# Kernel tuning notes

Hardware: AMD Instinct MI355X
Metric: run time of the kernel (lower is better)

Reference implementation:

```python
import jax, jax.numpy as jnp
import numpy as np

B, SQ, SK, D, H, DFF, L = 8, 1024, 1024, 512, 8, 2048, 2
HD = D // H  # head dim = 64
EPS = 1e-5


def _ln(x, g, b):
    mu = jnp.mean(x, axis=-1, keepdims=True)
    var = jnp.mean((x - mu) ** 2, axis=-1, keepdims=True)
    return (x - mu) * jax.lax.rsqrt(var + EPS) * g + b


def setup_inputs() -> dict:
    key = jax.random.key(0)
    ks = jax.random.split(key, 16)
    std = 0.02
    inp = {
        'q': jax.random.normal(ks[0], (B, SQ, D), jnp.float32),
        'k': jax.random.normal(ks[1], (B, SK, D), jnp.float32),
        'v': jax.random.normal(ks[2], (B, SK, D), jnp.float32),
        # per-layer stacked params (weights stored [in, out])
        'WQ': jax.random.normal(ks[3], (L, D, D), jnp.float32) * std,
        'bQ': jnp.zeros((L, D), jnp.float32),
        'WK': jax.random.normal(ks[4], (L, D, D), jnp.float32) * std,
        'bK': jnp.zeros((L, D), jnp.float32),
        'WV': jax.random.normal(ks[5], (L, D, D), jnp.float32) * std,
        'bV': jnp.zeros((L, D), jnp.float32),
        'WO': jax.random.normal(ks[6], (L, D, D), jnp.float32) * std,
        'bO': jnp.zeros((L, D), jnp.float32),
        'Wf1': jax.random.normal(ks[7], (L, D, DFF), jnp.float32) * std,
        'bf1': jnp.zeros((L, DFF), jnp.float32),
        'Wf2': jax.random.normal(ks[8], (L, DFF, D), jnp.float32) * std,
        'bf2': jnp.zeros((L, D), jnp.float32),
        'ln1_g': jnp.ones((L, D), jnp.float32),
        'ln1_b': jnp.zeros((L, D), jnp.float32),
        'ln2_g': jnp.ones((L, D), jnp.float32),
        'ln2_b': jnp.zeros((L, D), jnp.float32),
        'scale': jnp.full((L,), HD ** -0.5, jnp.float32),       # self.scale init
        'extra_scale': jnp.ones((L,), jnp.float32),             # self.extra_scale init
        'gate_attn': jnp.ones((L,), jnp.float32),
        'gate_ffn': jnp.ones((L,), jnp.float32),
    }
    return inp


def reference(q, k, v, WQ, bQ, WK, bK, WV, bV, WO, bO, Wf1, bf1, Wf2, bf2,
              ln1_g, ln1_b, ln2_g, ln2_b, scale, extra_scale, gate_attn, gate_ffn):
    prev = None  # Realformer residual attention scores
    for i in range(L):
        # QKV projections -> [B, H, S, HD]
        qh = (jnp.einsum('bsd,de->bse', q, WQ[i]) + bQ[i]).reshape(B, SQ, H, HD).transpose(0, 2, 1, 3)
        kh = (jnp.einsum('bsd,de->bse', k, WK[i]) + bK[i]).reshape(B, SK, H, HD).transpose(0, 2, 1, 3)
        vh = (jnp.einsum('bsd,de->bse', v, WV[i]) + bV[i]).reshape(B, SK, H, HD).transpose(0, 2, 1, 3)
        eff_scale = scale[i] * jnp.clip(extra_scale[i], 0.01, 50.0)
        scores = jnp.einsum('bhqd,bhkd->bhqk', qh, kh) * eff_scale  # [B,H,SQ,SK]
        if prev is not None:
            scores = scores + prev
        attn = jax.nn.softmax(scores, axis=-1)
        out = jnp.einsum('bhqk,bhkd->bhqd', attn, vh)
        out = out.transpose(0, 2, 1, 3).reshape(B, SQ, D)
        out = jnp.einsum('bsd,de->bse', out, WO[i]) + bO[i]
        # gated residual + post-norm
        q = q + jax.nn.softplus(gate_attn[i]) * out
        q = _ln(q, ln1_g[i], ln1_b[i])
        # FFN (exact gelu like torch default)
        ff = jax.nn.gelu(jnp.einsum('bsd,df->bsf', q, Wf1[i]) + bf1[i], approximate=False)
        ff = jnp.einsum('bsf,fd->bsd', ff, Wf2[i]) + bf2[i]
        q = q + jax.nn.softplus(gate_ffn[i]) * ff
        q = _ln(q, ln2_g[i], ln2_b[i])
        prev = scores
    return q
```

## Files before the change

### kernel.cpp

```cpp
#include <hip/hip_runtime.h>

#define B_   8
#define SQ_  1024
#define SK_  1024
#define D_   512
#define H_   8
#define DFF_ 2048
#define L_   2
#define HD_  64
#define M_   8192

typedef __bf16 bf16;
using bf16x8 = __attribute__((ext_vector_type(8))) __bf16;
using f32x4  = __attribute__((ext_vector_type(4))) float;

__device__ inline f32x4 mfma16(bf16x8 a, bf16x8 b, f32x4 c) {
  return __builtin_amdgcn_mfma_f32_16x16x32_bf16(a, b, c, 0, 0, 0);
}

__device__ __forceinline__ void gl2lds16(const bf16* g, bf16* l) {
  __builtin_amdgcn_global_load_lds(
      (const __attribute__((address_space(1))) void*)g,
      (__attribute__((address_space(3))) void*)l, 16, 0, 0);
}

__device__ __forceinline__ float gelu_fast(float x) {
  float u = 1.5957691216f * (x + 0.044715f * x * x * x);
  return x / (1.0f + __expf(-u));
}

struct TP4 { const float* in[4]; bf16* out[4]; };
__global__ __launch_bounds__(256) void transpose4_k(TP4 p) {
  __shared__ bf16 tile[32][33];
  int z = blockIdx.z, wsel = z >> 1, l = z & 1;
  const float* inp  = p.in[wsel]  + (size_t)l * D_ * D_;
  bf16*        outp = p.out[wsel] + (size_t)l * D_ * D_;
  int c0 = blockIdx.x * 32, r0 = blockIdx.y * 32;
  int tx = threadIdx.x & 31, ty = threadIdx.x >> 5;
#pragma unroll
  for (int i = 0; i < 32; i += 8)
    tile[ty + i][tx] = (bf16)inp[(size_t)(r0 + ty + i) * D_ + c0 + tx];
  __syncthreads();
#pragma unroll
  for (int i = 0; i < 32; i += 8)
    outp[(size_t)(c0 + ty + i) * D_ + r0 + tx] = tile[tx][ty + i];
}

__global__ __launch_bounds__(256) void transpose_k(
    const float* __restrict__ in, bf16* __restrict__ out, int R, int C) {
  __shared__ bf16 tile[32][33];
  const float* inp  = in  + (size_t)blockIdx.z * R * C;
  bf16*        outp = out + (size_t)blockIdx.z * R * C;
  int c0 = blockIdx.x * 32, r0 = blockIdx.y * 32;
  int tx = threadIdx.x & 31, ty = threadIdx.x >> 5;
#pragma unroll
  for (int i = 0; i < 32; i += 8)
    tile[ty + i][tx] = (bf16)inp[(size_t)(r0 + ty + i) * C + c0 + tx];
  __syncthreads();
#pragma unroll
  for (int i = 0; i < 32; i += 8)
    outp[(size_t)(c0 + ty + i) * R + r0 + tx] = tile[tx][ty + i];
}

__global__ __launch_bounds__(256) void f2b3_k(
    const float* __restrict__ a, const float* __restrict__ b,
    const float* __restrict__ c, bf16* __restrict__ oa,
    bf16* __restrict__ ob, bf16* __restrict__ oc) {
  int which = blockIdx.y;
  const float* in = (which == 0) ? a : (which == 1) ? b : c;
  bf16* out = (which == 0) ? oa : (which == 1) ? ob : oc;
  int i = (blockIdx.x * 256 + threadIdx.x) * 4;
  float4 v = *(const float4*)&in[i];
  out[i] = (bf16)v.x; out[i + 1] = (bf16)v.y;
  out[i + 2] = (bf16)v.z; out[i + 3] = (bf16)v.w;
}

struct G256 { const bf16* A; const bf16* Bt; const float* bias; bf16* C; };

#define MFB(mh) \
  _Pragma("unroll") \
  for (int mi = 0; mi < 4; mi++) { \
    _Pragma("unroll") \
    for (int ni = 0; ni < 4; ni++) \
      acc[(mh) * 4 + mi][ni] = mfma16(a[mi], b[ni], acc[(mh) * 4 + mi][ni]); \
  }

#define PHASE(s, mh, STAGE, VM) \
  { \
    if ((mh) == 0) { \
      a[0] = ldA(s, 0); a[1] = ldA(s, 1); a[2] = ldA(s, 2); a[3] = ldA(s, 3); \
      b[0] = ldB(s, 0); b[1] = ldB(s, 1); b[2] = ldB(s, 2); b[3] = ldB(s, 3); \
    } else { \
      a[0] = ldA(s, 4); a[1] = ldA(s, 5); a[2] = ldA(s, 6); a[3] = ldA(s, 7); \
    } \
    STAGE; \
    VM; \
    __builtin_amdgcn_s_barrier(); \
    asm volatile("s_waitcnt lgkmcnt(0)" ::: "memory"); \
    __builtin_amdgcn_sched_barrier(0); \
    __builtin_amdgcn_s_setprio(1); \
    MFB(mh); \
    __builtin_amdgcn_s_setprio(0); \
    __builtin_amdgcn_s_barrier(); \
  }

__global__ __launch_bounds__(512, 2) void gemm256_k(G256 g0, G256 g1,
                                                    int Nsz, int Ksz,
                                                    int gelu) {
  __shared__ bf16 As[4 * 8192];
  __shared__ bf16 Bs[4 * 8192];
  const G256 g = blockIdx.z ? g1 : g0;
  const int tid = threadIdx.x;
  const int w = tid >> 6, lane = tid & 63;
  const int quad = lane >> 4, l16 = lane & 15;
  const int wm = w >> 2, wn = w & 3;
  const int m0 = blockIdx.x * 256, n0 = blockIdx.y * 256;
  const int NCH = Ksz >> 5;
  const int ITERS = NCH >> 2;

  const int srow = tid >> 2;
  const int ssw = ((tid & 3) ^ (srow & 3) ^ ((srow >> 2) & 3)) << 3;
  const int swr = ((quad ^ (l16 & 3) ^ (l16 >> 2)) << 3);

  auto stageA = [&](int kc, int s) {
    const bf16* gp = g.A + (size_t)(m0 + srow) * Ksz + kc * 32 + ssw;
    gl2lds16(gp, &As[s * 8192 + w * 512]);
    gl2lds16(gp + (size_t)128 * Ksz, &As[s * 8192 + 4096 + w * 512]);
  };
  auto stageB = [&](int kc, int s) {
    const bf16* gp = g.Bt + (size_t)(n0 + srow) * Ksz + kc * 32 + ssw;
    gl2lds16(gp, &Bs[s * 8192 + w * 512]);
    gl2lds16(gp + (size_t)128 * Ksz, &Bs[s * 8192 + 4096 + w * 512]);
  };
  auto ldA = [&](int s, int mi) {
    return *(const bf16x8*)&As[s * 8192 + (wm * 128 + mi * 16 + l16) * 32 + swr];
  };
  auto ldB = [&](int s, int ni) {
    return *(const bf16x8*)&Bs[s * 8192 + (wn * 64 + ni * 16 + l16) * 32 + swr];
  };

  f32x4 acc[8][4] = {};

  stageA(0, 0); stageB(0, 0);
  stageA(1, 1); stageB(1, 1);
  stageA(2, 2); stageB(2, 2);
  asm volatile("s_waitcnt vmcnt(4)" ::: "memory");
  __builtin_amdgcn_s_barrier();

  for (int it = 0; it < ITERS; ++it) {
    const int c = it * 4;
    const bool last = (it + 1 == ITERS);
    bf16x8 a[4], b[4];
    PHASE(0, 0, stageA(c + 3, 3), )
    PHASE(0, 1, stageB(c + 3, 3), )
    PHASE(1, 0, if (!last) stageA(c + 4, 0), )
    PHASE(1, 1, if (!last) stageB(c + 4, 0),
          if (!last) { asm volatile("s_waitcnt vmcnt(4)" ::: "memory"); }
          else { asm volatile("s_waitcnt vmcnt(0)" ::: "memory"); })
    PHASE(2, 0, if (!last) stageA(c + 5, 1), )
    PHASE(2, 1, if (!last) stageB(c + 5, 1), )
    PHASE(3, 0, if (!last) stageA(c + 6, 2), )
    PHASE(3, 1, if (!last) stageB(c + 6, 2),
          asm volatile("s_waitcnt vmcnt(4)" ::: "memory"))
  }

#pragma unroll
  for (int mi = 0; mi < 8; mi++)
#pragma unroll
    for (int ni = 0; ni < 4; ni++) {
      const int col = n0 + wn * 64 + ni * 16 + l16;
      const float bv = g.bias[col];
#pragma unroll
      for (int r = 0; r < 4; r++) {
        const int row = m0 + wm * 128 + mi * 16 + quad * 4 + r;
        float x = acc[mi][ni][r] + bv;
        if (gelu) x = gelu_fast(x);
        g.C[(size_t)row * Nsz + col] = (bf16)x;
      }
    }
}

__global__ __launch_bounds__(512, 2) void gemm128_k(
    const bf16* __restrict__ A, const bf16* __restrict__ Bt,
    const float* __restrict__ bias, bf16* __restrict__ Cb,
    float* __restrict__ Cf, int Nsz, int Ksz) {
  __shared__ bf16 As[4 * 4096];
  __shared__ bf16 Bs[4 * 4096];
  const int tid = threadIdx.x;
  const int w = tid >> 6, lane = tid & 63;
  const int quad = lane >> 4, l16 = lane & 15;
  const int wm = w >> 2, wn = w & 3;
  const int m0 = blockIdx.x * 128, n0 = blockIdx.y * 128;
  const int NCH = Ksz >> 5;

  const int srow = tid >> 2;
  const int ssw = ((tid & 3) ^ (srow & 3) ^ ((srow >> 2) & 3)) << 3;
  const int swr = ((quad ^ (l16 & 3) ^ (l16 >> 2)) << 3);

  auto stageChunk = [&](int kc) {
    const int s = kc & 3;
    gl2lds16(A + (size_t)(m0 + srow) * Ksz + kc * 32 + ssw,
             &As[s * 4096 + w * 512]);
    gl2lds16(Bt + (size_t)(n0 + srow) * Ksz + kc * 32 + ssw,
             &Bs[s * 4096 + w * 512]);
  };
  auto ldA = [&](int s, int mi) {
    return *(const bf16x8*)&As[s * 4096 + (wm * 64 + mi * 16 + l16) * 32 + swr];
  };
  auto ldB = [&](int s, int ni) {
    return *(const bf16x8*)&Bs[s * 4096 + (wn * 32 + ni * 16 + l16) * 32 + swr];
  };

  f32x4 acc[4][2] = {};

  stageChunk(0); stageChunk(1); stageChunk(2);
  asm volatile("s_waitcnt vmcnt(4)" ::: "memory");
  __builtin_amdgcn_s_barrier();

  auto phase = [&](int c, int vml) {
    const int s = c & 3;
    if (vml == 4) stageChunk(c + 3);
    bf16x8 a0 = ldA(s, 0), a1 = ldA(s, 1), a2 = ldA(s, 2), a3 = ldA(s, 3);
    bf16x8 b0 = ldB(s, 0), b1 = ldB(s, 1);
    if (vml == 4)      asm volatile("s_waitcnt vmcnt(4)" ::: "memory");
    else if (vml == 2) asm volatile("s_waitcnt vmcnt(2)" ::: "memory");
    else if (vml == 0) asm volatile("s_waitcnt vmcnt(0)" ::: "memory");
    __builtin_amdgcn_s_barrier();
    asm volatile("s_waitcnt lgkmcnt(0)" ::: "memory");
    __builtin_amdgcn_sched_barrier(0);
    __builtin_amdgcn_s_setprio(1);
    acc[0][0] = mfma16(a0, b0, acc[0][0]);
    acc[0][1] = mfma16(a0, b1, acc[0][1]);
    acc[1][0] = mfma16(a1, b0, acc[1][0]);
    acc[1][1] = mfma16(a1, b1, acc[1][1]);
    acc[2][0] = mfma16(a2, b0, acc[2][0]);
    acc[2][1] = mfma16(a2, b1, acc[2][1]);
    acc[3][0] = mfma16(a3, b0, acc[3][0]);
    acc[3][1] = mfma16(a3, b1, acc[3][1]);
    __builtin_amdgcn_s_setprio(0);
    __builtin_amdgcn_s_barrier();
  };

  for (int c = 0; c + 4 <= NCH; ++c) phase(c, 4);
  phase(NCH - 3, 2);
  phase(NCH - 2, 0);
  phase(NCH - 1, -1);

#pragma unroll
  for (int mi = 0; mi < 4; mi++)
#pragma unroll
    for (int ni = 0; ni < 2; ni++) {
      const int col = n0 + wn * 32 + ni * 16 + l16;
      const float bv = bias[col];
#pragma unroll
      for (int r = 0; r < 4; r++) {
        const int row = m0 + wm * 64 + mi * 16 + quad * 4 + r;
        float x = acc[mi][ni][r] + bv;
        size_t idx = (size_t)row * Nsz + col;
        if (Cb) Cb[idx] = (bf16)x;
        if (Cf) Cf[idx] = x;
      }
    }
}

__global__ __launch_bounds__(256) void vtrans2_k(const bf16* __restrict__ vhh,
                                                 bf16* __restrict__ vt0,
                                                 bf16* __restrict__ vt1) {
  __shared__ bf16 sm[64][72];
  int kt = blockIdx.x, bh = blockIdx.y, z = blockIdx.z;
  int coloff = z ? D_ : 0;
  bf16* vt = z ? vt1 : vt0;
  int b = bh >> 3, h = bh & 7;
  int tid = threadIdx.x;
  for (int c = tid; c < 512; c += 256) {
    int key = c >> 3, off = (c & 7) * 8;
    *(uint4*)&sm[key][off] = *(const uint4*)
        &vhh[(size_t)(b * SK_ + kt * 64 + key) * (2 * D_) + coloff + h * 64 + off];
  }
  __syncthreads();
  for (int c = tid; c < 512; c += 256) {
    int hd = c >> 3, koff = (c & 7) * 8;
    bf16 tmp[8];
#pragma unroll
    for (int j = 0; j < 8; j++) tmp[j] = sm[koff + j][hd];
    *(uint4*)&vt[(size_t)(bh * 64 + hd) * SK_ + kt * 64 + koff] = *(uint4*)tmp;
  }
}

template<bool HAS0>
__global__ __launch_bounds__(256) void attn_t(
    const bf16* __restrict__ qh, const bf16* __restrict__ qh0,
    const bf16* __restrict__ kh, const bf16* __restrict__ kh0, int kstride,
    const bf16* __restrict__ vt, const float* __restrict__ scale,
    const float* __restrict__ extra, int li, bf16* __restrict__ ctx) {
  __shared__ bf16 Ks[2 * 2 * 2048];
  __shared__ bf16 K0s[HAS0 ? 2 * 2 * 2048 : 64];
  __shared__ bf16 Vs[2 * 2 * 2048];
  __shared__ bf16 Ps[4][16 * 72];
  int qt = blockIdx.x, bh = blockIdx.y;
  int b = bh >> 3, h = bh & 7;
  int tid = threadIdx.x, w = tid >> 6, lane = tid & 63;
  int quad = lane >> 4, l16 = lane & 15;
  const int r4 = lane >> 2, c4 = (lane & 3) * 8;
  float eff1 = scale[li] * fminf(fmaxf(extra[li], 0.01f), 50.0f);
  float eff0 = HAS0 ? scale[li - 1] * fminf(fmaxf(extra[li - 1], 0.01f), 50.0f) : 0.f;
  bf16x8 aq[2][2], aq0[2][2];
#pragma unroll
  for (int mi = 0; mi < 2; mi++) {
    int qrow = b * SQ_ + qt * 128 + w * 32 + mi * 16 + l16;
    const bf16* qp = qh + (size_t)qrow * D_ + h * 64 + quad * 8;
    aq[mi][0] = *(const bf16x8*)qp; aq[mi][1] = *(const bf16x8*)(qp + 32);
#pragma unroll
    for (int k2 = 0; k2 < 2; k2++)
#pragma unroll
      for (int j = 0; j < 8; j++)
        aq[mi][k2][j] = (bf16)((float)aq[mi][k2][j] * eff1);
    if constexpr (HAS0) {
      const bf16* qp0 = qh0 + (size_t)qrow * D_ + h * 64 + quad * 8;
      aq0[mi][0] = *(const bf16x8*)qp0; aq0[mi][1] = *(const bf16x8*)(qp0 + 32);
#pragma unroll
      for (int k2 = 0; k2 < 2; k2++)
#pragma unroll
        for (int j = 0; j < 8; j++)
          aq0[mi][k2][j] = (bf16)((float)aq0[mi][k2][j] * eff0);
    }
  }
  bf16x8 ones;
#pragma unroll
  for (int j = 0; j < 8; j++) ones[j] = (bf16)1.0f;

  f32x4 o[2][4] = {};
  f32x4 ol[2] = {};

  auto stage = [&](int kt, int bufi) {
    size_t kg = (size_t)(b * SK_ + kt * 64 + w * 16 + r4) * kstride + h * 64 + c4;
    gl2lds16(&kh[kg],      &Ks[(bufi * 2 + 0) * 2048 + (w * 16) * 32]);
    gl2lds16(&kh[kg + 32], &Ks[(bufi * 2 + 1) * 2048 + (w * 16) * 32]);
    if constexpr (HAS0) {
      gl2lds16(&kh0[kg],      &K0s[(bufi * 2 + 0) * 2048 + (w * 16) * 32]);
      gl2lds16(&kh0[kg + 32], &K0s[(bufi * 2 + 1) * 2048 + (w * 16) * 32]);
    }
    size_t vg = (size_t)(bh * 64 + w * 16 + r4) * SK_ + kt * 64 + c4;
    gl2lds16(&vt[vg],      &Vs[(bufi * 2 + 0) * 2048 + (w * 16) * 32]);
    gl2lds16(&vt[vg + 32], &Vs[(bufi * 2 + 1) * 2048 + (w * 16) * 32]);
  };

  stage(0, 0);
  __syncthreads();
  int buf = 0;
  for (int kt = 0; kt < SK_ / 64; kt++, buf ^= 1) {
    if (kt + 1 < SK_ / 64) stage(kt + 1, buf ^ 1);
    bf16x8 bv[2][4];
#pragma unroll
    for (int kk = 0; kk < 2; kk++)
#pragma unroll
      for (int ni = 0; ni < 4; ni++)
        bv[kk][ni] = *(const bf16x8*)&Vs[kk * 2048 + buf * 4096 +
                                         (ni * 16 + l16) * 32 + quad * 8];
#pragma unroll
    for (int mi = 0; mi < 2; mi++) {
#pragma unroll
      for (int ni = 0; ni < 4; ni++) {
        int ro = (ni * 16 + l16) * 32 + quad * 8;
        f32x4 t = {};
        t = mfma16(aq[mi][0], *(const bf16x8*)&Ks[0 * 2048 + buf * 4096 + ro], t);
        t = mfma16(aq[mi][1], *(const bf16x8*)&Ks[1 * 2048 + buf * 4096 + ro], t);
        if constexpr (HAS0) {
          t = mfma16(aq0[mi][0], *(const bf16x8*)&K0s[0 * 2048 + buf * 4096 + ro], t);
          t = mfma16(aq0[mi][1], *(const bf16x8*)&K0s[1 * 2048 + buf * 4096 + ro], t);
        }
#pragma unroll
        for (int r = 0; r < 4; r++)
          Ps[w][(quad * 4 + r) * 72 + ni * 16 + l16] = (bf16)__expf(t[r]);
      }
#pragma unroll
      for (int kk = 0; kk < 2; kk++) {
        bf16x8 ap = *(const bf16x8*)&Ps[w][l16 * 72 + kk * 32 + quad * 8];
        ol[mi] = mfma16(ap, ones, ol[mi]);
#pragma unroll
        for (int ni = 0; ni < 4; ni++)
          o[mi][ni] = mfma16(ap, bv[kk][ni], o[mi][ni]);
      }
    }
    __syncthreads();
  }
#pragma unroll
  for (int mi = 0; mi < 2; mi++)
#pragma unroll
    for (int ni = 0; ni < 4; ni++)
#pragma unroll
      for (int r = 0; r < 4; r++) {
        int row = b * SQ_ + qt * 128 + w * 32 + mi * 16 + quad * 4 + r;
        ctx[(size_t)row * D_ + h * 64 + ni * 16 + l16] =
            (bf16)(o[mi][ni][r] / ol[mi][r]);
      }
}

__global__ __launch_bounds__(256) void ln_k(
    const float* __restrict__ cur_in, const float* __restrict__ add,
    const float* __restrict__ gate, const float* __restrict__ g,
    const float* __restrict__ bb, float* __restrict__ outf,
    bf16* __restrict__ outb) {
  int row = blockIdx.x, tid = threadIdx.x;
  float gv = gate[0];
  float sp = gv > 20.f ? gv : log1pf(expf(gv));
  size_t base = (size_t)row * D_;
  int c0 = tid * 2;
  float2 c2 = *(const float2*)&cur_in[base + c0];
  float2 a2 = *(const float2*)&add[base + c0];
  float x0 = c2.x + sp * a2.x, x1 = c2.y + sp * a2.y;
  float s = x0 + x1, s2 = x0 * x0 + x1 * x1;
#pragma unroll
  for (int m = 1; m < 64; m <<= 1) {
    s += __shfl_xor(s, m);
    s2 += __shfl_xor(s2, m);
  }
  __shared__ float sa[4], sb[4];
  int w = tid >> 6;
  if ((tid & 63) == 0) { sa[w] = s; sb[w] = s2; }
  __syncthreads();
  s = sa[0] + sa[1] + sa[2] + sa[3];
  s2 = sb[0] + sb[1] + sb[2] + sb[3];
  float mu = s * (1.f / D_);
  float var = s2 * (1.f / D_) - mu * mu;
  float rs = rsqrtf(var + 1e-5f);
  float y0 = (x0 - mu) * rs * g[c0] + bb[c0];
  float y1 = (x1 - mu) * rs * g[c0 + 1] + bb[c0 + 1];
  if (outf) { float2 y; y.x = y0; y.y = y1; *(float2*)&outf[base + c0] = y; }
  if (outb) { outb[base + c0] = (bf16)y0; outb[base + c0 + 1] = (bf16)y1; }
}

extern "C" void kernel_launch(void* const* d_in, const int* in_sizes, int n_in,
                              void* d_out, int out_size, void* d_ws,
                              size_t ws_size, hipStream_t stream) {
  const float* qin = (const float*)d_in[0];
  const float* kin = (const float*)d_in[1];
  const float* vin = (const float*)d_in[2];
  const float* WQ  = (const float*)d_in[3];
  const float* bQ  = (const float*)d_in[4];
  const float* WK  = (const float*)d_in[5];
  const float* bK  = (const float*)d_in[6];
  const float* WV  = (const float*)d_in[7];
  const float* bV  = (const float*)d_in[8];
  const float* WO  = (const float*)d_in[9];
  const float* bO  = (const float*)d_in[10];
  const float* Wf1 = (const float*)d_in[11];
  const float* bf1 = (const float*)d_in[12];
  const float* Wf2 = (const float*)d_in[13];
  const float* bf2 = (const float*)d_in[14];
  const float* l1g = (const float*)d_in[15];
  const float* l1b = (const float*)d_in[16];
  const float* l2g = (const float*)d_in[17];
  const float* l2b = (const float*)d_in[18];
  const float* sc  = (const float*)d_in[19];
  const float* ex  = (const float*)d_in[20];
  const float* ga  = (const float*)d_in[21];
  const float* gf  = (const float*)d_in[22];

  char* p = (char*)d_ws;
  auto alloc = [&](size_t bytes) {
    void* r = (void*)p;
    p += (bytes + 255) & ~(size_t)255;
    return r;
  };
  bf16* WQt  = (bf16*)alloc((size_t)L_ * D_ * D_ * 2);
  bf16* WKt  = (bf16*)alloc((size_t)L_ * D_ * D_ * 2);
  bf16* WVt  = (bf16*)alloc((size_t)L_ * D_ * D_ * 2);
  bf16* WOt  = (bf16*)alloc((size_t)L_ * D_ * D_ * 2);
  bf16* Wf1t = (bf16*)alloc((size_t)L_ * D_ * DFF_ * 2);
  bf16* Wf2t = (bf16*)alloc((size_t)L_ * D_ * DFF_ * 2);
  float* cur  = (float*)alloc((size_t)M_ * D_ * 4);
  bf16* curb  = (bf16*)alloc((size_t)M_ * D_ * 2);
  bf16* qb    = (bf16*)alloc((size_t)M_ * D_ * 2);
  bf16* kb    = (bf16*)alloc((size_t)M_ * D_ * 2);
  bf16* vb    = (bf16*)alloc((size_t)M_ * D_ * 2);
  bf16* khh   = (bf16*)alloc((size_t)M_ * 2 * D_ * 2);
  bf16* vhh   = (bf16*)alloc((size_t)M_ * 2 * D_ * 2);
  bf16* qh0b  = (bf16*)alloc((size_t)M_ * D_ * 2);
  bf16* qh1b  = (bf16*)alloc((size_t)M_ * D_ * 2);
  bf16* vt0   = (bf16*)alloc((size_t)M_ * D_ * 2);
  bf16* vt1   = (bf16*)alloc((size_t)M_ * D_ * 2);
  bf16* ctx   = (bf16*)alloc((size_t)M_ * D_ * 2);
  float* proj = (float*)alloc((size_t)M_ * D_ * 4);
  bf16* ffmid = (bf16*)alloc((size_t)M_ * DFF_ * 2);
  float* ffout = (float*)alloc((size_t)M_ * D_ * 4);

  TP4 tp; tp.in[0] = WQ; tp.in[1] = WK; tp.in[2] = WV; tp.in[3] = WO;
  tp.out[0] = WQt; tp.out[1] = WKt; tp.out[2] = WVt; tp.out[3] = WOt;
  transpose4_k<<<dim3(16, 16, 8), 256, 0, stream>>>(tp);
  transpose_k<<<dim3(DFF_ / 32, D_ / 32, L_), 256, 0, stream>>>(Wf1, Wf1t, D_, DFF_);
  transpose_k<<<dim3(D_ / 32, DFF_ / 32, L_), 256, 0, stream>>>(Wf2, Wf2t, DFF_, D_);
  f2b3_k<<<dim3((M_ * D_) / 1024, 3), 256, 0, stream>>>(qin, kin, vin, qb, kb, vb);

  G256 gk; gk.A = kb; gk.Bt = WKt; gk.bias = bK; gk.C = khh;
  G256 gvv; gvv.A = vb; gvv.Bt = WVt; gvv.bias = bV; gvv.C = vhh;
  gemm256_k<<<dim3(M_ / 256, (2 * D_) / 256, 2), 512, 0, stream>>>(
      gk, gvv, 2 * D_, D_, 0);
  vtrans2_k<<<dim3(SK_ / 64, B_ * H_, 2), 256, 0, stream>>>(vhh, vt0, vt1);
  gemm128_k<<<dim3(M_ / 128, 4), 512, 0, stream>>>(
      qb, WQt, bQ, qh0b, nullptr, D_, D_);

  for (int li = 0; li < L_; li++) {
    if (li > 0)
      gemm128_k<<<dim3(M_ / 128, 4), 512, 0, stream>>>(
          curb, WQt + (size_t)li * D_ * D_, bQ + li * D_, qh1b, nullptr, D_, D_);
    if (li == 0)
      attn_t<false><<<dim3(SQ_ / 128, B_ * H_), 256, 0, stream>>>(
          qh0b, qh0b, khh, khh, 2 * D_, vt0, sc, ex, 0, ctx);
    else
      attn_t<true><<<dim3(SQ_ / 128, B_ * H_), 256, 0, stream>>>(
          qh1b, qh0b, khh + (size_t)li * D_, khh, 2 * D_, vt1, sc, ex, 1, ctx);
    gemm128_k<<<dim3(M_ / 128, 4), 512, 0, stream>>>(
        ctx, WOt + (size_t)li * D_ * D_, bO + li * D_, nullptr, proj, D_, D_);
    ln_k<<<M_, 256, 0, stream>>>((li == 0) ? qin : cur, proj, ga + li,
                                 l1g + li * D_, l1b + li * D_, cur, curb);
    G256 gf1; gf1.A = curb; gf1.Bt = Wf1t + (size_t)li * D_ * DFF_;
    gf1.bias = bf1 + li * DFF_; gf1.C = ffmid;
    gemm256_k<<<dim3(M_ / 256, DFF_ / 256, 1), 512, 0, stream>>>(
        gf1, gf1, DFF_, D_, 1);
    gemm128_k<<<dim3(M_ / 128, 4), 512, 0, stream>>>(
        ffmid, Wf2t + (size_t)li * DFF_ * D_, bf2 + li * D_, nullptr, ffout,
        D_, DFF_);
    ln_k<<<M_, 256, 0, stream>>>(cur, ffout, gf + li, l2g + li * D_,
                                 l2b + li * D_,
                                 (li == L_ - 1) ? (float*)d_out : cur,
                                 (li == L_ - 1) ? nullptr : curb);
  }
}
```

Before: 534.9 us.

## Split-K the FFN down-projection with 256 tiles, swizzle attention LDS, add setprio

```diff
diff --git a/kernel.cpp b/kernel.cpp
--- a/kernel.cpp
+++ b/kernel.cpp
@@ -176,6 +176,81 @@
         float x = acc[mi][ni][r] + bv;
         if (gelu) x = gelu_fast(x);
         g.C[(size_t)row * Nsz + col] = (bf16)x;
+      }
+    }
+}
+
+__global__ __launch_bounds__(512, 2) void gemm256s_k(
+    const bf16* __restrict__ A, const bf16* __restrict__ Bt,
+    bf16* __restrict__ P, int Nsz, int Kstride, int Kpart) {
+  __shared__ bf16 As[4 * 8192];
+  __shared__ bf16 Bs[4 * 8192];
+  const int z = blockIdx.z;
+  const int koff = z * Kpart;
+  const int tid = threadIdx.x;
+  const int w = tid >> 6, lane = tid & 63;
+  const int quad = lane >> 4, l16 = lane & 15;
+  const int wm = w >> 2, wn = w & 3;
+  const int m0 = blockIdx.x * 256, n0 = blockIdx.y * 256;
+  const int ITERS = (Kpart >> 5) >> 2;
+
+  const int srow = tid >> 2;
+  const int ssw = ((tid & 3) ^ (srow & 3) ^ ((srow >> 2) & 3)) << 3;
+  const int swr = ((quad ^ (l16 & 3) ^ (l16 >> 2)) << 3);
+
+  auto stageA = [&](int kc, int s) {
+    const bf16* gp = A + (size_t)(m0 + srow) * Kstride + koff + kc * 32 + ssw;
+    gl2lds16(gp, &As[s * 8192 + w * 512]);
+    gl2lds16(gp + (size_t)128 * Kstride, &As[s * 8192 + 4096 + w * 512]);
+  };
+  auto stageB = [&](int kc, int s) {
+    const bf16* gp = Bt + (size_t)(n0 + srow) * Kstride + koff + kc * 32 + ssw;
+    gl2lds16(gp, &Bs[s * 8192 + w * 512]);
+    gl2lds16(gp + (size_t)128 * Kstride, &Bs[s * 8192 + 4096 + w * 512]);
+  };
+  auto ldA = [&](int s, int mi) {
+    return *(const bf16x8*)&As[s * 8192 + (wm * 128 + mi * 16 + l16) * 32 + swr];
+  };
+  auto ldB = [&](int s, int ni) {
+    return *(const bf16x8*)&Bs[s * 8192 + (wn * 64 + ni * 16 + l16) * 32 + swr];
+  };
+
+  f32x4 acc[8][4] = {};
+
+  stageA(0, 0); stageB(0, 0);
+  stageA(1, 1); stageB(1, 1);
+  stageA(2, 2); stageB(2, 2);
+  asm volatile("s_waitcnt vmcnt(4)" ::: "memory");
+  __builtin_amdgcn_s_barrier();
+
+  for (int it = 0; it < ITERS; ++it) {
+    const int c = it * 4;
+    const bool last = (it + 1 == ITERS);
+    bf16x8 a[4], b[4];
+    PHASE(0, 0, stageA(c + 3, 3), )
+    PHASE(0, 1, stageB(c + 3, 3), )
+    PHASE(1, 0, if (!last) stageA(c + 4, 0), )
+    PHASE(1, 1, if (!last) stageB(c + 4, 0),
+          if (!last) { asm volatile("s_waitcnt vmcnt(4)" ::: "memory"); }
+          else { asm volatile("s_waitcnt vmcnt(0)" ::: "memory"); })
+    PHASE(2, 0, if (!last) stageA(c + 5, 1), )
+    PHASE(2, 1, if (!last) stageB(c + 5, 1), )
+    PHASE(3, 0, if (!last) stageA(c + 6, 2), )
+    PHASE(3, 1, if (!last) stageB(c + 6, 2),
+          asm volatile("s_waitcnt vmcnt(4)" ::: "memory"))
+  }
+
+  const size_t Msz = (size_t)gridDim.x * 256;
+  bf16* Pz = P + (size_t)z * Msz * Nsz;
+#pragma unroll
+  for (int mi = 0; mi < 8; mi++)
+#pragma unroll
+    for (int ni = 0; ni < 4; ni++) {
+      const int col = n0 + wn * 64 + ni * 16 + l16;
+#pragma unroll
+      for (int r = 0; r < 4; r++) {
+        const int row = m0 + wm * 128 + mi * 16 + quad * 4 + r;
+        Pz[(size_t)row * Nsz + col] = (bf16)acc[mi][ni][r];
       }
     }
 }
@@ -301,7 +376,9 @@
   int b = bh >> 3, h = bh & 7;
   int tid = threadIdx.x, w = tid >> 6, lane = tid & 63;
   int quad = lane >> 4, l16 = lane & 15;
-  const int r4 = lane >> 2, c4 = (lane & 3) * 8;
+  const int r4 = lane >> 2;
+  const int c4s = (((lane & 3) ^ (r4 & 3) ^ ((r4 >> 2) & 3))) * 8;
+  const int swr = ((quad ^ (l16 & 3) ^ (l16 >> 2)) << 3);
   float eff1 = scale[li] * fminf(fmaxf(extra[li], 0.01f), 50.0f);
   float eff0 = HAS0 ? scale[li - 1] * fminf(fmaxf(extra[li - 1], 0.01f), 50.0f) : 0.f;
   bf16x8 aq[2][2], aq0[2][2];
@@ -333,14 +410,14 @@
   f32x4 ol[2] = {};
 
   auto stage = [&](int kt, int bufi) {
-    size_t kg = (size_t)(b * SK_ + kt * 64 + w * 16 + r4) * kstride + h * 64 + c4;
+    size_t kg = (size_t)(b * SK_ + kt * 64 + w * 16 + r4) * kstride + h * 64 + c4s;
     gl2lds16(&kh[kg],      &Ks[(bufi * 2 + 0) * 2048 + (w * 16) * 32]);
     gl2lds16(&kh[kg + 32], &Ks[(bufi * 2 + 1) * 2048 + (w * 16) * 32]);
     if constexpr (HAS0) {
       gl2lds16(&kh0[kg],      &K0s[(bufi * 2 + 0) * 2048 + (w * 16) * 32]);
       gl2lds16(&kh0[kg + 32], &K0s[(bufi * 2 + 1) * 2048 + (w * 16) * 32]);
     }
-    size_t vg = (size_t)(bh * 64 + w * 16 + r4) * SK_ + kt * 64 + c4;
+    size_t vg = (size_t)(bh * 64 + w * 16 + r4) * SK_ + kt * 64 + c4s;
     gl2lds16(&vt[vg],      &Vs[(bufi * 2 + 0) * 2048 + (w * 16) * 32]);
     gl2lds16(&vt[vg + 32], &Vs[(bufi * 2 + 1) * 2048 + (w * 16) * 32]);
   };
@@ -356,19 +433,21 @@
 #pragma unroll
       for (int ni = 0; ni < 4; ni++)
         bv[kk][ni] = *(const bf16x8*)&Vs[kk * 2048 + buf * 4096 +
-                                         (ni * 16 + l16) * 32 + quad * 8];
+                                         (ni * 16 + l16) * 32 + swr];
 #pragma unroll
     for (int mi = 0; mi < 2; mi++) {
 #pragma unroll
       for (int ni = 0; ni < 4; ni++) {
-        int ro = (ni * 16 + l16) * 32 + quad * 8;
+        int ro = (ni * 16 + l16) * 32 + swr;
         f32x4 t = {};
+        __builtin_amdgcn_s_setprio(1);
         t = mfma16(aq[mi][0], *(const bf16x8*)&Ks[0 * 2048 + buf * 4096 + ro], t);
         t = mfma16(aq[mi][1], *(const bf16x8*)&Ks[1 * 2048 + buf * 4096 + ro], t);
         if constexpr (HAS0) {
           t = mfma16(aq0[mi][0], *(const bf16x8*)&K0s[0 * 2048 + buf * 4096 + ro], t);
           t = mfma16(aq0[mi][1], *(const bf16x8*)&K0s[1 * 2048 + buf * 4096 + ro], t);
         }
+        __builtin_amdgcn_s_setprio(0);
 #pragma unroll
         for (int r = 0; r < 4; r++)
           Ps[w][(quad * 4 + r) * 72 + ni * 16 + l16] = (bf16)__expf(t[r]);
@@ -376,10 +455,12 @@
 #pragma unroll
       for (int kk = 0; kk < 2; kk++) {
         bf16x8 ap = *(const bf16x8*)&Ps[w][l16 * 72 + kk * 32 + quad * 8];
+        __builtin_amdgcn_s_setprio(1);
         ol[mi] = mfma16(ap, ones, ol[mi]);
 #pragma unroll
         for (int ni = 0; ni < 4; ni++)
           o[mi][ni] = mfma16(ap, bv[kk][ni], o[mi][ni]);
+        __builtin_amdgcn_s_setprio(0);
       }
     }
     __syncthreads();
@@ -409,6 +490,47 @@
   float2 c2 = *(const float2*)&cur_in[base + c0];
   float2 a2 = *(const float2*)&add[base + c0];
   float x0 = c2.x + sp * a2.x, x1 = c2.y + sp * a2.y;
+  float s = x0 + x1, s2 = x0 * x0 + x1 * x1;
+#pragma unroll
+  for (int m = 1; m < 64; m <<= 1) {
+    s += __shfl_xor(s, m);
+    s2 += __shfl_xor(s2, m);
+  }
+  __shared__ float sa[4], sb[4];
+  int w = tid >> 6;
+  if ((tid & 63) == 0) { sa[w] = s; sb[w] = s2; }
+  __syncthreads();
+  s = sa[0] + sa[1] + sa[2] + sa[3];
+  s2 = sb[0] + sb[1] + sb[2] + sb[3];
+  float mu = s * (1.f / D_);
+  float var = s2 * (1.f / D_) - mu * mu;
+  float rs = rsqrtf(var + 1e-5f);
+  float y0 = (x0 - mu) * rs * g[c0] + bb[c0];
+  float y1 = (x1 - mu) * rs * g[c0 + 1] + bb[c0 + 1];
+  if (outf) { float2 y; y.x = y0; y.y = y1; *(float2*)&outf[base + c0] = y; }
+  if (outb) { outb[base + c0] = (bf16)y0; outb[base + c0 + 1] = (bf16)y1; }
+}
+
+__global__ __launch_bounds__(256) void ln4_k(
+    const float* __restrict__ cur_in, const bf16* __restrict__ P,
+    const float* __restrict__ bias2, const float* __restrict__ gate,
+    const float* __restrict__ g, const float* __restrict__ bb,
+    float* __restrict__ outf, bf16* __restrict__ outb) {
+  int row = blockIdx.x, tid = threadIdx.x;
+  float gv = gate[0];
+  float sp = gv > 20.f ? gv : log1pf(expf(gv));
+  size_t base = (size_t)row * D_;
+  int c0 = tid * 2;
+  float2 c2 = *(const float2*)&cur_in[base + c0];
+  float a0 = bias2[c0], a1 = bias2[c0 + 1];
+  const size_t MD = (size_t)M_ * D_;
+#pragma unroll
+  for (int z = 0; z < 4; z++) {
+    const bf16* pp = P + z * MD + base + c0;
+    a0 += (float)pp[0];
+    a1 += (float)pp[1];
+  }
+  float x0 = c2.x + sp * a0, x1 = c2.y + sp * a1;
   float s = x0 + x1, s2 = x0 * x0 + x1 * x1;
 #pragma unroll
   for (int m = 1; m < 64; m <<= 1) {
@@ -481,9 +603,11 @@
   bf16* vt0   = (bf16*)alloc((size_t)M_ * D_ * 2);
   bf16* vt1   = (bf16*)alloc((size_t)M_ * D_ * 2);
   bf16* ctx   = (bf16*)alloc((size_t)M_ * D_ * 2);
-  float* proj = (float*)alloc((size_t)M_ * D_ * 4);
-  bf16* ffmid = (bf16*)alloc((size_t)M_ * DFF_ * 2);
+  float* proj  = (float*)alloc((size_t)M_ * D_ * 4);
   float* ffout = (float*)alloc((size_t)M_ * D_ * 4);
+  bf16* parts  = (bf16*)proj;
+  bf16* ffmid  = (bf16*)alloc((size_t)M_ * DFF_ * 2);
+  (void)ffout;
 
   TP4 tp; tp.in[0] = WQ; tp.in[1] = WK; tp.in[2] = WV; tp.in[3] = WO;
   tp.out[0] = WQt; tp.out[1] = WKt; tp.out[2] = WVt; tp.out[3] = WOt;
@@ -518,12 +642,11 @@
     gf1.bias = bf1 + li * DFF_; gf1.C = ffmid;
     gemm256_k<<<dim3(M_ / 256, DFF_ / 256, 1), 512, 0, stream>>>(
         gf1, gf1, DFF_, D_, 1);
-    gemm128_k<<<dim3(M_ / 128, 4), 512, 0, stream>>>(
-        ffmid, Wf2t + (size_t)li * DFF_ * D_, bf2 + li * D_, nullptr, ffout,
-        D_, DFF_);
-    ln_k<<<M_, 256, 0, stream>>>(cur, ffout, gf + li, l2g + li * D_,
-                                 l2b + li * D_,
-                                 (li == L_ - 1) ? (float*)d_out : cur,
-                                 (li == L_ - 1) ? nullptr : curb);
-  }
-}
+    gemm256s_k<<<dim3(M_ / 256, D_ / 256, 4), 512, 0, stream>>>(
+        ffmid, Wf2t + (size_t)li * DFF_ * D_, parts, D_, DFF_, DFF_ / 4);
+    ln4_k<<<M_, 256, 0, stream>>>(cur, parts, bf2 + li * D_, gf + li,
+                                  l2g + li * D_, l2b + li * D_,
+                                  (li == L_ - 1) ? (float*)d_out : cur,
+                                  (li == L_ - 1) ? nullptr : curb);
+  }
+}
```

Measured after the change: 506.7 us. 5.3% less time.
